# Kernel optimization log

Measured on AMD Instinct MI355X. Metric: run time of the kernel, lower is better.

Reference implementation:

```python
import jax, jax.numpy as jnp
import numpy as np

N_NODES = 50000
N_EDGES = 1600000
N_GRAPHS = 64


def setup_inputs() -> dict:
    key = jax.random.key(0)
    ks = jax.random.split(key, 16)
    x = jax.random.normal(ks[0], (N_NODES, 900), dtype=jnp.float32)
    edge_index = jax.random.randint(ks[1], (2, N_EDGES), 0, N_NODES, dtype=jnp.int64)
    batch = jnp.sort(jax.random.randint(ks[2], (N_NODES,), 0, N_GRAPHS, dtype=jnp.int64))

    def lin(k, out_d, in_d):
        return jax.random.normal(k, (out_d, in_d), dtype=jnp.float32) / np.sqrt(in_d)

    return {
        "x": x, "edge_index": edge_index, "batch": batch,
        # SAGEConv1: lin_l (aggregated, with bias), lin_r (root, no bias)
        "W1l": lin(ks[3], 1024, 900), "b1": jnp.zeros((1024,), jnp.float32), "W1r": lin(ks[4], 1024, 900),
        # SAGEConv2
        "W2l": lin(ks[5], 2048, 1024), "b2": jnp.zeros((2048,), jnp.float32), "W2r": lin(ks[6], 2048, 1024),
        # MLP head
        "Wf1": lin(ks[7], 1024, 2048), "bf1": jnp.zeros((1024,), jnp.float32),
        "Wf2": lin(ks[8], 6, 1024), "bf2": jnp.zeros((6,), jnp.float32),
    }


def _sage_conv(x, src, dst, Wl, b, Wr):
    # mean aggregation of neighbor (source) features onto target nodes
    agg = jax.ops.segment_sum(x[src], dst, num_segments=N_NODES)
    deg = jax.ops.segment_sum(jnp.ones((src.shape[0],), x.dtype), dst, num_segments=N_NODES)
    mean = agg / jnp.maximum(deg, 1.0)[:, None]
    return mean @ Wl.T + b + x @ Wr.T


def reference(x, edge_index, batch, W1l, b1, W1r, W2l, b2, W2r, Wf1, bf1, Wf2, bf2):
    src, dst = edge_index[0], edge_index[1]
    h = jax.nn.relu(_sage_conv(x, src, dst, W1l, b1, W1r))   # [N, 1024]
    h = _sage_conv(h, src, dst, W2l, b2, W2r)                 # [N, 2048]
    pooled = jax.ops.segment_max(h, batch, num_segments=N_GRAPHS)  # [G, 2048]
    pooled = jnp.where(jnp.isfinite(pooled), pooled, 0.0)     # guard empty graphs
    out = jax.nn.relu(pooled @ Wf1.T + bf1) @ Wf2.T + bf2     # [G, 6]
    return out
```

## Files before the change

kernel.cpp:

```cpp
#include <hip/hip_runtime.h>

typedef unsigned short u16x8 __attribute__((ext_vector_type(8)));
typedef char i8x16 __attribute__((ext_vector_type(16)));
typedef int i32x4 __attribute__((ext_vector_type(4)));

constexpr int NN = 50000;
constexpr int NG = 64;
constexpr int MP = 50048;
constexpr int D0 = 900;
constexpr int K0 = 960;
constexpr int D1 = 1024;
constexpr int D2 = 2048;

__device__ __forceinline__ float bf2f(unsigned short u) {
  return __uint_as_float(((unsigned)u) << 16);
}
__device__ __forceinline__ unsigned short f2bf(float f) {
  unsigned x = __float_as_uint(f);
  return (unsigned short)((x + 0x7fffu + ((x >> 16) & 1u)) >> 16);
}

__device__ __forceinline__ void gl_lds16(const void* g, void* l) {
  __builtin_amdgcn_global_load_lds((const __attribute__((address_space(1))) void*)g,
                                   (__attribute__((address_space(3))) void*)l, 16, 0, 0);
}

__global__ __launch_bounds__(256) void cvt_x(const float* __restrict__ in,
                                             char* __restrict__ xi8,
                                             float* __restrict__ xscale) {
  int r = blockIdx.x;
  __shared__ float row[K0];
  __shared__ float smax[256];
  int t = threadIdx.x;
  float m = 0.f;
  for (int c = t; c < K0; c += 256) {
    float v = (r < NN && c < D0) ? in[(size_t)r * D0 + c] : 0.f;
    row[c] = v;
    m = fmaxf(m, fabsf(v));
  }
  smax[t] = m;
  __syncthreads();
  for (int dd = 128; dd; dd >>= 1) {
    if (t < dd) smax[t] = fmaxf(smax[t], smax[t + dd]);
    __syncthreads();
  }
  float mx = smax[0];
  float inv = mx > 0.f ? 127.f / mx : 0.f;
  for (int c = t; c < K0; c += 256) xi8[(size_t)r * K0 + c] = (char)(int)rintf(row[c] * inv);
  if (t == 0) xscale[r] = mx * (1.f / 127.f);
}

__global__ __launch_bounds__(256) void wq_k(const float* __restrict__ in, int Cin, int KP,
                                            char* __restrict__ q, float* __restrict__ sc) {
  int r = blockIdx.x;
  __shared__ float smax[256];
  int t = threadIdx.x;
  float m = 0.f;
  for (int c = t; c < Cin; c += 256) m = fmaxf(m, fabsf(in[(size_t)r * Cin + c]));
  smax[t] = m;
  __syncthreads();
  for (int dd = 128; dd; dd >>= 1) {
    if (t < dd) smax[t] = fmaxf(smax[t], smax[t + dd]);
    __syncthreads();
  }
  float mx = smax[0];
  float inv = mx > 0.f ? 127.f / mx : 0.f;
  for (int c = t; c < KP; c += 256) {
    float v = (c < Cin) ? in[(size_t)r * Cin + c] : 0.f;
    q[(size_t)r * KP + c] = (char)(int)rintf(v * inv);
  }
  if (t == 0) sc[r] = mx * (1.f / 127.f);
}

__global__ __launch_bounds__(256) void quant_rows(const unsigned short* __restrict__ in,
                                                  char* __restrict__ q,
                                                  float* __restrict__ scale, int K) {
  int r = blockIdx.x;
  __shared__ float row[1024];
  __shared__ float smax[256];
  int t = threadIdx.x;
  float m = 0.f;
  for (int c = t; c < K; c += 256) {
    float v = bf2f(in[(size_t)r * K + c]);
    row[c] = v;
    m = fmaxf(m, fabsf(v));
  }
  smax[t] = m;
  __syncthreads();
  for (int dd = 128; dd; dd >>= 1) {
    if (t < dd) smax[t] = fmaxf(smax[t], smax[t + dd]);
    __syncthreads();
  }
  float mx = smax[0];
  float inv = mx > 0.f ? 127.f / mx : 0.f;
  for (int c = t; c < K; c += 256) q[(size_t)r * K + c] = (char)(int)rintf(row[c] * inv);
  if (t == 0) scale[r] = mx * (1.f / 127.f);
}

__global__ void zero_i(int* p, int n) {
  int i = blockIdx.x * blockDim.x + threadIdx.x;
  if (i < n) p[i] = 0;
}
__global__ void count_k(const int* __restrict__ dst, int* __restrict__ deg, int E, int n) {
  int e = blockIdx.x * blockDim.x + threadIdx.x;
  if (e < E) {
    int d = dst[e];
    if ((unsigned)d < (unsigned)n) atomicAdd(&deg[d], 1);
  }
}
__global__ void scan_k(const int* __restrict__ deg, int* __restrict__ off, int n) {
  __shared__ int s[1024];
  __shared__ int carry;
  int t = threadIdx.x;
  if (t == 0) carry = 0;
  __syncthreads();
  for (int base = 0; base < n; base += 1024) {
    int v = (base + t < n) ? deg[base + t] : 0;
    s[t] = v;
    __syncthreads();
    for (int d = 1; d < 1024; d <<= 1) {
      int x = (t >= d) ? s[t - d] : 0;
      __syncthreads();
      s[t] += x;
      __syncthreads();
    }
    if (base + t < n) off[base + t] = carry + s[t] - v;
    int total = s[1023];
    __syncthreads();
    if (t == 0) carry += total;
    __syncthreads();
  }
  if (t == 0) off[n] = carry;
}
__global__ void copy_i(const int* a, int* b, int n) {
  int i = blockIdx.x * blockDim.x + threadIdx.x;
  if (i < n) b[i] = a[i];
}
__global__ void fill_k(const int* __restrict__ src, const int* __restrict__ dst,
                       int* __restrict__ cursor, int* __restrict__ csr, int E, int n) {
  int e = blockIdx.x * blockDim.x + threadIdx.x;
  if (e < E) {
    int d = dst[e];
    if ((unsigned)d < (unsigned)n) {
      int p = atomicAdd(&cursor[d], 1);
      int s = src[e];
      if ((unsigned)s >= (unsigned)n) s = 0;
      csr[p] = s;
    }
  }
}

template <int K>
__global__ __launch_bounds__(256) void agg_mean_i8q(const char* __restrict__ feat,
                                                    const float* __restrict__ scale,
                                                    const int* __restrict__ off,
                                                    const int* __restrict__ csr,
                                                    char* __restrict__ mean_i8,
                                                    float* __restrict__ smean) {
  __shared__ float red[3][1024];
  const int node = blockIdx.x;
  const int wave = threadIdx.x >> 6, lane = threadIdx.x & 63;
  const int d = lane * 16;
  const bool act = (d < K);
  const int e0 = off[node], e1 = off[node + 1];
  float a[16];
#pragma unroll
  for (int k = 0; k < 16; ++k) a[k] = 0.f;
  if (act) {
    const char* fp = feat + d;
    int e = e0 + wave;
    for (; e + 12 < e1; e += 16) {
      int s0 = csr[e], s1 = csr[e + 4], s2 = csr[e + 8], s3 = csr[e + 12];
      float c0 = scale[s0], c1 = scale[s1], c2 = scale[s2], c3 = scale[s3];
      i8x16 v0 = *(const i8x16*)(fp + (size_t)s0 * K);
      i8x16 v1 = *(const i8x16*)(fp + (size_t)s1 * K);
      i8x16 v2 = *(const i8x16*)(fp + (size_t)s2 * K);
      i8x16 v3 = *(const i8x16*)(fp + (size_t)s3 * K);
#pragma unroll
      for (int k = 0; k < 16; ++k) {
        a[k] += c0 * (float)v0[k];
        a[k] += c1 * (float)v1[k];
        a[k] += c2 * (float)v2[k];
        a[k] += c3 * (float)v3[k];
      }
    }
    for (; e < e1; e += 4) {
      int s = csr[e];
      float c = scale[s];
      i8x16 v = *(const i8x16*)(fp + (size_t)s * K);
#pragma unroll
      for (int k = 0; k < 16; ++k) a[k] += c * (float)v[k];
    }
  }
  if (wave > 0 && act) {
#pragma unroll
    for (int k = 0; k < 16; ++k) red[wave - 1][d + k] = a[k];
  }
  __syncthreads();
  if (wave == 0) {
    int deg = e1 - e0;
    float inv = 1.f / (float)(deg > 1 ? deg : 1);
    float m[16];
    float mx = 0.f;
    if (act) {
#pragma unroll
      for (int k = 0; k < 16; ++k) {
        m[k] = (a[k] + red[0][d + k] + red[1][d + k] + red[2][d + k]) * inv;
        mx = fmaxf(mx, fabsf(m[k]));
      }
    }
    for (int o = 32; o; o >>= 1) mx = fmaxf(mx, __shfl_down(mx, o));
    mx = __shfl(mx, 0);
    if (lane == 0) smean[node] = mx * (1.f / 127.f);
    float qi = mx > 0.f ? 127.f / mx : 0.f;
    if (act) {
      i8x16 q;
#pragma unroll
      for (int k = 0; k < 16; ++k) q[k] = (char)(int)rintf(m[k] * qi);
      *(i8x16*)&mean_i8[(size_t)node * K + d] = q;
    }
  }
}

__device__ __forceinline__ void kloop_i8(const char* __restrict__ gA,
                                         const char* __restrict__ gW,
                                         char* lA, char* lB, char* sA, char* sB, int KP,
                                         i32x4 (&iacc)[4][4], int wm, int wn, int l16,
                                         int quad) {
#pragma unroll 1
  for (int k0 = 0; k0 < KP; k0 += 64) {
    __syncthreads();
    gl_lds16(gA + k0, lA);
    gl_lds16(gA + k0 + (size_t)64 * KP, lA + 4096);
    gl_lds16(gW + k0, lB);
    gl_lds16(gW + k0 + (size_t)64 * KP, lB + 4096);
    __syncthreads();
    i32x4 af[4], bg[4];
#pragma unroll
    for (int i = 0; i < 4; ++i)
      af[i] = *(const i32x4*)&sA[(wm + 16 * i + l16) * 64 + quad * 16];
#pragma unroll
    for (int j = 0; j < 4; ++j)
      bg[j] = *(const i32x4*)&sB[(wn + 16 * j + l16) * 64 + quad * 16];
#pragma unroll
    for (int i = 0; i < 4; ++i)
#pragma unroll
      for (int j = 0; j < 4; ++j)
        iacc[i][j] = __builtin_amdgcn_mfma_i32_16x16x64_i8(af[i], bg[j], iacc[i][j], 0, 0, 0);
  }
}

template <int KP, int N, bool RELU>
__global__ __launch_bounds__(256) void gemm_i8_dual(
    const char* __restrict__ A1, const char* __restrict__ W1,
    const char* __restrict__ A2, const char* __restrict__ W2,
    const float* __restrict__ sA1, const float* __restrict__ sW1,
    const float* __restrict__ sA2, const float* __restrict__ sW2,
    const float* __restrict__ bias, unsigned short* __restrict__ C) {
  __shared__ char sA[128 * 64];
  __shared__ char sB[128 * 64];
  __shared__ float sc0[128], sc1[128], sc2[128], sc3[128];
  const int tid = threadIdx.x;
  const int wave = tid >> 6, lane = tid & 63;
  const int quad = lane >> 4, l16 = lane & 15;
  const int wm = (wave >> 1) * 64, wn = (wave & 1) * 64;
  const long long bm = (long long)blockIdx.y * 128;
  const long long bn = (long long)blockIdx.x * 128;

  if (tid < 128) {
    sc0[tid] = sA1[bm + tid];
    sc2[tid] = sA2[bm + tid];
  } else {
    sc1[tid - 128] = sW1[bn + tid - 128];
    sc3[tid - 128] = sW2[bn + tid - 128];
  }

  const int srow = wave * 16 + (lane >> 2);
  const int skoff = (lane & 3) * 16;
  char* lA = &sA[wave * 1024 + lane * 16];
  char* lB = &sB[wave * 1024 + lane * 16];

  i32x4 iacc[4][4];
#pragma unroll
  for (int i = 0; i < 4; ++i)
#pragma unroll
    for (int j = 0; j < 4; ++j) iacc[i][j] = (i32x4){0, 0, 0, 0};

  kloop_i8(A1 + (bm + srow) * (long long)KP + skoff, W1 + (bn + srow) * (long long)KP + skoff,
           lA, lB, sA, sB, KP, iacc, wm, wn, l16, quad);

  unsigned int fb[4][4][2];
#pragma unroll
  for (int i = 0; i < 4; ++i) {
    const int rowb = wm + 16 * i + quad * 4;
#pragma unroll
    for (int j = 0; j < 4; ++j) {
      const float cw = sc1[wn + 16 * j + l16];
      float v0 = (float)iacc[i][j][0] * sc0[rowb + 0] * cw;
      float v1 = (float)iacc[i][j][1] * sc0[rowb + 1] * cw;
      float v2 = (float)iacc[i][j][2] * sc0[rowb + 2] * cw;
      float v3 = (float)iacc[i][j][3] * sc0[rowb + 3] * cw;
      fb[i][j][0] = (unsigned)f2bf(v0) | ((unsigned)f2bf(v1) << 16);
      fb[i][j][1] = (unsigned)f2bf(v2) | ((unsigned)f2bf(v3) << 16);
      iacc[i][j] = (i32x4){0, 0, 0, 0};
    }
  }

  kloop_i8(A2 + (bm + srow) * (long long)KP + skoff, W2 + (bn + srow) * (long long)KP + skoff,
           lA, lB, sA, sB, KP, iacc, wm, wn, l16, quad);

#pragma unroll
  for (int j = 0; j < 4; ++j) {
    const int coll = wn + 16 * j + l16;
    const long long col = bn + coll;
    const float bv = bias[col];
    const float cw2 = sc3[coll];
#pragma unroll
    for (int i = 0; i < 4; ++i) {
      const int rowb = wm + 16 * i + quad * 4;
      const long long row0 = bm + rowb;
#pragma unroll
      for (int r = 0; r < 4; ++r) {
        float p1 = bf2f((unsigned short)(fb[i][j][r >> 1] >> ((r & 1) * 16)));
        float v = p1 + (float)iacc[i][j][r] * sc2[rowb + r] * cw2 + bv;
        if (RELU) v = fmaxf(v, 0.f);
        C[(row0 + r) * (long long)N + col] = f2bf(v);
      }
    }
  }
}

__global__ void bounds_k(const int* __restrict__ batch, int* __restrict__ gstart, int n, int G) {
  int g = blockIdx.x * blockDim.x + threadIdx.x;
  if (g > G) return;
  int lo = 0, hi = n;
  while (lo < hi) {
    int mid = (lo + hi) >> 1;
    if (batch[mid] < g) lo = mid + 1; else hi = mid;
  }
  gstart[g] = lo;
}

__global__ void segmax_k(const unsigned short* __restrict__ h2b, const int* __restrict__ gstart,
                         float* __restrict__ pooled) {
  int g = blockIdx.x;
  int c = blockIdx.y * 256 + threadIdx.x;
  int i0 = gstart[g], i1 = gstart[g + 1];
  float m = -3.4e38f;
  for (int i = i0; i < i1; ++i) m = fmaxf(m, bf2f(h2b[(size_t)i * D2 + c]));
  if (i0 >= i1) m = 0.f;
  pooled[(size_t)g * D2 + c] = m;
}

__global__ void head1_k(const float* __restrict__ pooled, const float* __restrict__ Wf1,
                        const float* __restrict__ bf1, float* __restrict__ hid) {
  int g = blockIdx.x, chunk = blockIdx.y;
  __shared__ float sp[2048];
  for (int i = threadIdx.x; i < 2048; i += 256) sp[i] = pooled[(size_t)g * 2048 + i];
  __syncthreads();
  int wave = threadIdx.x >> 6, lane = threadIdx.x & 63;
  for (int oi = wave; oi < 64; oi += 4) {
    int o = chunk * 64 + oi;
    const float4* wr = (const float4*)&Wf1[(size_t)o * 2048];
    float s = 0.f;
    for (int c = lane; c < 512; c += 64) {
      float4 wv = wr[c];
      float4 pv = *(const float4*)&sp[c * 4];
      s += wv.x * pv.x + wv.y * pv.y + wv.z * pv.z + wv.w * pv.w;
    }
    for (int off = 32; off; off >>= 1) s += __shfl_down(s, off);
    if (lane == 0) hid[(size_t)g * 1024 + o] = fmaxf(s + bf1[o], 0.f);
  }
}
__global__ void head2_k(const float* __restrict__ hid, const float* __restrict__ Wf2,
                        const float* __restrict__ bf2, float* __restrict__ out) {
  int g = blockIdx.x, t = threadIdx.x;
  __shared__ float sh[1024];
  __shared__ float red[256];
  for (int i = t; i < 1024; i += 256) sh[i] = hid[(size_t)g * 1024 + i];
  __syncthreads();
  for (int o = 0; o < 6; ++o) {
    float s = 0.f;
    for (int k = t; k < 1024; k += 256) s += sh[k] * Wf2[o * 1024 + k];
    red[t] = s;
    __syncthreads();
    for (int d = 128; d; d >>= 1) {
      if (t < d) red[t] += red[t + d];
      __syncthreads();
    }
    if (t == 0) out[g * 6 + o] = red[0] + bf2[o];
    __syncthreads();
  }
}

extern "C" void kernel_launch(void* const* d_in, const int* in_sizes, int n_in,
                              void* d_out, int out_size, void* d_ws, size_t ws_size,
                              hipStream_t stream) {
  const float* x    = (const float*)d_in[0];
  const int* ei     = (const int*)d_in[1];
  const int* batch  = (const int*)d_in[2];
  const float* W1l  = (const float*)d_in[3];
  const float* b1   = (const float*)d_in[4];
  const float* W1r  = (const float*)d_in[5];
  const float* W2l  = (const float*)d_in[6];
  const float* b2   = (const float*)d_in[7];
  const float* W2r  = (const float*)d_in[8];
  const float* Wf1  = (const float*)d_in[9];
  const float* bf1  = (const float*)d_in[10];
  const float* Wf2  = (const float*)d_in[11];
  const float* bf2  = (const float*)d_in[12];
  float* out = (float*)d_out;

  const int E = in_sizes[1] / 2;
  const int* srcp = ei;
  const int* dstp = ei + E;

  char* w = (char*)d_ws;
  auto take = [&](size_t b) {
    void* p = (void*)w;
    w += (b + 255) & ~(size_t)255;
    return p;
  };
  char* xi8       = (char*)take((size_t)MP * K0);
  char* mean_i8   = (char*)take((size_t)MP * K0);
  char* h1_i8     = (char*)take((size_t)MP * D1);
  char* mean2_i8  = (char*)take((size_t)MP * D1);
  unsigned short* h1b = (unsigned short*)take((size_t)MP * D1 * 2);
  unsigned short* h2b = (unsigned short*)take((size_t)MP * D2 * 2);
  char* w1l_i8    = (char*)take((size_t)D1 * K0);
  char* w1r_i8    = (char*)take((size_t)D1 * K0);
  char* w2l_i8    = (char*)take((size_t)D2 * D1);
  char* w2r_i8    = (char*)take((size_t)D2 * D1);
  float* xscale   = (float*)take((size_t)MP * 4);
  float* smean    = (float*)take((size_t)MP * 4);
  float* h1scale  = (float*)take((size_t)MP * 4);
  float* smean2   = (float*)take((size_t)MP * 4);
  float* sW1l     = (float*)take((size_t)D1 * 4);
  float* sW1r     = (float*)take((size_t)D1 * 4);
  float* sW2l     = (float*)take((size_t)D2 * 4);
  float* sW2r     = (float*)take((size_t)D2 * 4);
  int* deg    = (int*)take((size_t)MP * 4);
  int* off    = (int*)take((size_t)(MP + 1) * 4);
  int* cursor = (int*)take((size_t)MP * 4);
  int* csr    = (int*)take((size_t)E * 4);
  int* gstart = (int*)take((size_t)(NG + 1) * 4);
  float* pooled = (float*)take((size_t)NG * D2 * 4);
  float* hid    = (float*)take((size_t)NG * 1024 * 4);

  cvt_x<<<MP, 256, 0, stream>>>(x, xi8, xscale);
  wq_k<<<D1, 256, 0, stream>>>(W1l, D0, K0, w1l_i8, sW1l);
  wq_k<<<D1, 256, 0, stream>>>(W1r, D0, K0, w1r_i8, sW1r);
  wq_k<<<D2, 256, 0, stream>>>(W2l, D1, D1, w2l_i8, sW2l);
  wq_k<<<D2, 256, 0, stream>>>(W2r, D1, D1, w2r_i8, sW2r);

  zero_i<<<(MP + 255) / 256, 256, 0, stream>>>(deg, MP);
  count_k<<<(E + 255) / 256, 256, 0, stream>>>(dstp, deg, E, NN);
  scan_k<<<1, 1024, 0, stream>>>(deg, off, MP);
  copy_i<<<(MP + 255) / 256, 256, 0, stream>>>(off, cursor, MP);
  fill_k<<<(E + 255) / 256, 256, 0, stream>>>(srcp, dstp, cursor, csr, E, NN);

  agg_mean_i8q<K0><<<MP, 256, 0, stream>>>(xi8, xscale, off, csr, mean_i8, smean);
  gemm_i8_dual<K0, D1, true><<<dim3(D1 / 128, MP / 128), 256, 0, stream>>>(
      mean_i8, w1l_i8, xi8, w1r_i8, smean, sW1l, xscale, sW1r, b1, h1b);

  quant_rows<<<MP, 256, 0, stream>>>(h1b, h1_i8, h1scale, D1);
  agg_mean_i8q<D1><<<MP, 256, 0, stream>>>(h1_i8, h1scale, off, csr, mean2_i8, smean2);
  gemm_i8_dual<D1, D2, false><<<dim3(D2 / 128, MP / 128), 256, 0, stream>>>(
      mean2_i8, w2l_i8, h1_i8, w2r_i8, smean2, sW2l, h1scale, sW2r, b2, h2b);

  bounds_k<<<1, 128, 0, stream>>>(batch, gstart, NN, NG);
  segmax_k<<<dim3(NG, D2 / 256), 256, 0, stream>>>(h2b, gstart, pooled);
  head1_k<<<dim3(NG, 16), 256, 0, stream>>>(pooled, Wf1, bf1, hid);
  head2_k<<<NG, 256, 0, stream>>>(hid, Wf2, bf2, out);
}
```

Baseline: 2.002 ms.

## Concatenate mean and root features into one int8 GEMM with shared scales

```diff
diff --git a/kernel.cpp b/kernel.cpp
--- a/kernel.cpp
+++ b/kernel.cpp
@@ -11,6 +11,8 @@
 constexpr int K0 = 960;
 constexpr int D1 = 1024;
 constexpr int D2 = 2048;
+constexpr int KC1 = 2 * K0;
+constexpr int KC2 = 2 * D1;
 
 __device__ __forceinline__ float bf2f(unsigned short u) {
   return __uint_as_float(((unsigned)u) << 16);
@@ -26,7 +28,7 @@
 }
 
 __global__ __launch_bounds__(256) void cvt_x(const float* __restrict__ in,
-                                             char* __restrict__ xi8,
+                                             char* __restrict__ cat1,
                                              float* __restrict__ xscale) {
   int r = blockIdx.x;
   __shared__ float row[K0];
@@ -46,17 +48,50 @@
   }
   float mx = smax[0];
   float inv = mx > 0.f ? 127.f / mx : 0.f;
-  for (int c = t; c < K0; c += 256) xi8[(size_t)r * K0 + c] = (char)(int)rintf(row[c] * inv);
+  char* dst = cat1 + (size_t)r * KC1 + K0;
+  for (int c = t; c < K0; c += 256) dst[c] = (char)(int)rintf(row[c] * inv);
   if (t == 0) xscale[r] = mx * (1.f / 127.f);
 }
 
-__global__ __launch_bounds__(256) void wq_k(const float* __restrict__ in, int Cin, int KP,
-                                            char* __restrict__ q, float* __restrict__ sc) {
+__global__ __launch_bounds__(256) void wq_cat(const float* __restrict__ Wl,
+                                              const float* __restrict__ Wr, int Cin, int KH,
+                                              char* __restrict__ q, float* __restrict__ sc) {
+  int r = blockIdx.x, t = threadIdx.x;
+  __shared__ float smax[256];
+  float m = 0.f;
+  for (int c = t; c < Cin; c += 256) {
+    m = fmaxf(m, fabsf(Wl[(size_t)r * Cin + c]));
+    m = fmaxf(m, fabsf(Wr[(size_t)r * Cin + c]));
+  }
+  smax[t] = m;
+  __syncthreads();
+  for (int dd = 128; dd; dd >>= 1) {
+    if (t < dd) smax[t] = fmaxf(smax[t], smax[t + dd]);
+    __syncthreads();
+  }
+  float mx = smax[0];
+  float inv = mx > 0.f ? 127.f / mx : 0.f;
+  char* row = q + (size_t)r * 2 * KH;
+  for (int c = t; c < KH; c += 256) {
+    row[c]      = (c < Cin) ? (char)(int)rintf(Wl[(size_t)r * Cin + c] * inv) : 0;
+    row[KH + c] = (c < Cin) ? (char)(int)rintf(Wr[(size_t)r * Cin + c] * inv) : 0;
+  }
+  if (t == 0) sc[r] = mx * (1.f / 127.f);
+}
+
+__global__ __launch_bounds__(256) void quant_rows(const unsigned short* __restrict__ in,
+                                                  char* __restrict__ cat2,
+                                                  float* __restrict__ scale) {
   int r = blockIdx.x;
+  __shared__ float row[D1];
   __shared__ float smax[256];
   int t = threadIdx.x;
   float m = 0.f;
-  for (int c = t; c < Cin; c += 256) m = fmaxf(m, fabsf(in[(size_t)r * Cin + c]));
+  for (int c = t; c < D1; c += 256) {
+    float v = bf2f(in[(size_t)r * D1 + c]);
+    row[c] = v;
+    m = fmaxf(m, fabsf(v));
+  }
   smax[t] = m;
   __syncthreads();
   for (int dd = 128; dd; dd >>= 1) {
@@ -65,35 +100,8 @@
   }
   float mx = smax[0];
   float inv = mx > 0.f ? 127.f / mx : 0.f;
-  for (int c = t; c < KP; c += 256) {
-    float v = (c < Cin) ? in[(size_t)r * Cin + c] : 0.f;
-    q[(size_t)r * KP + c] = (char)(int)rintf(v * inv);
-  }
-  if (t == 0) sc[r] = mx * (1.f / 127.f);
-}
-
-__global__ __launch_bounds__(256) void quant_rows(const unsigned short* __restrict__ in,
-                                                  char* __restrict__ q,
-                                                  float* __restrict__ scale, int K) {
-  int r = blockIdx.x;
-  __shared__ float row[1024];
-  __shared__ float smax[256];
-  int t = threadIdx.x;
-  float m = 0.f;
-  for (int c = t; c < K; c += 256) {
-    float v = bf2f(in[(size_t)r * K + c]);
-    row[c] = v;
-    m = fmaxf(m, fabsf(v));
-  }
-  smax[t] = m;
-  __syncthreads();
-  for (int dd = 128; dd; dd >>= 1) {
-    if (t < dd) smax[t] = fmaxf(smax[t], smax[t + dd]);
-    __syncthreads();
-  }
-  float mx = smax[0];
-  float inv = mx > 0.f ? 127.f / mx : 0.f;
-  for (int c = t; c < K; c += 256) q[(size_t)r * K + c] = (char)(int)rintf(row[c] * inv);
+  char* dst = cat2 + (size_t)r * KC2 + D1;
+  for (int c = t; c < D1; c += 256) dst[c] = (char)(int)rintf(row[c] * inv);
   if (t == 0) scale[r] = mx * (1.f / 127.f);
 }
 
@@ -108,29 +116,42 @@
     if ((unsigned)d < (unsigned)n) atomicAdd(&deg[d], 1);
   }
 }
-__global__ void scan_k(const int* __restrict__ deg, int* __restrict__ off, int n) {
-  __shared__ int s[1024];
-  __shared__ int carry;
+__global__ void scan1_k(const int* __restrict__ deg, int* __restrict__ off,
+                        int* __restrict__ bsum, int n) {
+  __shared__ int s[256];
   int t = threadIdx.x;
-  if (t == 0) carry = 0;
-  __syncthreads();
-  for (int base = 0; base < n; base += 1024) {
-    int v = (base + t < n) ? deg[base + t] : 0;
-    s[t] = v;
-    __syncthreads();
-    for (int d = 1; d < 1024; d <<= 1) {
-      int x = (t >= d) ? s[t - d] : 0;
-      __syncthreads();
-      s[t] += x;
-      __syncthreads();
-    }
-    if (base + t < n) off[base + t] = carry + s[t] - v;
-    int total = s[1023];
-    __syncthreads();
-    if (t == 0) carry += total;
-    __syncthreads();
-  }
-  if (t == 0) off[n] = carry;
+  int gid = blockIdx.x * 256 + t;
+  int v = (gid < n) ? deg[gid] : 0;
+  s[t] = v;
+  __syncthreads();
+  for (int d = 1; d < 256; d <<= 1) {
+    int x = (t >= d) ? s[t - d] : 0;
+    __syncthreads();
+    s[t] += x;
+    __syncthreads();
+  }
+  if (gid < n) off[gid] = s[t] - v;
+  if (t == 255) bsum[blockIdx.x] = s[255];
+}
+__global__ void scan2_k(int* __restrict__ bsum, int nb) {
+  __shared__ int s[256];
+  int t = threadIdx.x;
+  int v = (t < nb) ? bsum[t] : 0;
+  s[t] = v;
+  __syncthreads();
+  for (int d = 1; d < 256; d <<= 1) {
+    int x = (t >= d) ? s[t - d] : 0;
+    __syncthreads();
+    s[t] += x;
+    __syncthreads();
+  }
+  if (t < nb) bsum[t] = s[t] - v;
+  if (t == 255) bsum[nb] = s[255];
+}
+__global__ void scan3_k(int* __restrict__ off, const int* __restrict__ bsum, int n, int nb) {
+  int gid = blockIdx.x * 256 + threadIdx.x;
+  if (gid < n) off[gid] += bsum[gid >> 8];
+  if (gid == 0) off[n] = bsum[nb];
 }
 __global__ void copy_i(const int* a, int* b, int n) {
   int i = blockIdx.x * blockDim.x + threadIdx.x;
@@ -150,16 +171,13 @@
   }
 }
 
-template <int K>
-__global__ __launch_bounds__(256) void agg_mean_i8q(const char* __restrict__ feat,
-                                                    const float* __restrict__ scale,
+template <int K, int STRIDE>
+__global__ __launch_bounds__(256) void agg_mean_i8w(char* __restrict__ cat,
+                                                    const float* __restrict__ rscale,
                                                     const int* __restrict__ off,
-                                                    const int* __restrict__ csr,
-                                                    char* __restrict__ mean_i8,
-                                                    float* __restrict__ smean) {
-  __shared__ float red[3][1024];
-  const int node = blockIdx.x;
-  const int wave = threadIdx.x >> 6, lane = threadIdx.x & 63;
+                                                    const int* __restrict__ csr) {
+  const int node = blockIdx.x * 4 + (threadIdx.x >> 6);
+  const int lane = threadIdx.x & 63;
   const int d = lane * 16;
   const bool act = (d < K);
   const int e0 = off[node], e1 = off[node + 1];
@@ -167,99 +185,61 @@
 #pragma unroll
   for (int k = 0; k < 16; ++k) a[k] = 0.f;
   if (act) {
-    const char* fp = feat + d;
-    int e = e0 + wave;
-    for (; e + 12 < e1; e += 16) {
-      int s0 = csr[e], s1 = csr[e + 4], s2 = csr[e + 8], s3 = csr[e + 12];
-      float c0 = scale[s0], c1 = scale[s1], c2 = scale[s2], c3 = scale[s3];
-      i8x16 v0 = *(const i8x16*)(fp + (size_t)s0 * K);
-      i8x16 v1 = *(const i8x16*)(fp + (size_t)s1 * K);
-      i8x16 v2 = *(const i8x16*)(fp + (size_t)s2 * K);
-      i8x16 v3 = *(const i8x16*)(fp + (size_t)s3 * K);
+    const char* fp = cat + (size_t)K + d;
+    int e = e0;
+    for (; e + 7 < e1; e += 8) {
+      int s0 = csr[e],     s1 = csr[e + 1], s2 = csr[e + 2], s3 = csr[e + 3];
+      int s4 = csr[e + 4], s5 = csr[e + 5], s6 = csr[e + 6], s7 = csr[e + 7];
+      i8x16 v0 = *(const i8x16*)(fp + (size_t)s0 * STRIDE);
+      i8x16 v1 = *(const i8x16*)(fp + (size_t)s1 * STRIDE);
+      i8x16 v2 = *(const i8x16*)(fp + (size_t)s2 * STRIDE);
+      i8x16 v3 = *(const i8x16*)(fp + (size_t)s3 * STRIDE);
+      i8x16 v4 = *(const i8x16*)(fp + (size_t)s4 * STRIDE);
+      i8x16 v5 = *(const i8x16*)(fp + (size_t)s5 * STRIDE);
+      i8x16 v6 = *(const i8x16*)(fp + (size_t)s6 * STRIDE);
+      i8x16 v7 = *(const i8x16*)(fp + (size_t)s7 * STRIDE);
+      float c0 = rscale[s0], c1 = rscale[s1], c2 = rscale[s2], c3 = rscale[s3];
+      float c4 = rscale[s4], c5 = rscale[s5], c6 = rscale[s6], c7 = rscale[s7];
 #pragma unroll
       for (int k = 0; k < 16; ++k) {
-        a[k] += c0 * (float)v0[k];
-        a[k] += c1 * (float)v1[k];
-        a[k] += c2 * (float)v2[k];
-        a[k] += c3 * (float)v3[k];
+        a[k] += c0 * (float)v0[k] + c1 * (float)v1[k] + c2 * (float)v2[k] + c3 * (float)v3[k];
+        a[k] += c4 * (float)v4[k] + c5 * (float)v5[k] + c6 * (float)v6[k] + c7 * (float)v7[k];
       }
     }
-    for (; e < e1; e += 4) {
+    for (; e < e1; ++e) {
       int s = csr[e];
-      float c = scale[s];
-      i8x16 v = *(const i8x16*)(fp + (size_t)s * K);
+      float c = rscale[s];
+      i8x16 v = *(const i8x16*)(fp + (size_t)s * STRIDE);
 #pragma unroll
       for (int k = 0; k < 16; ++k) a[k] += c * (float)v[k];
     }
   }
-  if (wave > 0 && act) {
-#pragma unroll
-    for (int k = 0; k < 16; ++k) red[wave - 1][d + k] = a[k];
-  }
-  __syncthreads();
-  if (wave == 0) {
+  if (act) {
     int deg = e1 - e0;
     float inv = 1.f / (float)(deg > 1 ? deg : 1);
-    float m[16];
-    float mx = 0.f;
-    if (act) {
-#pragma unroll
-      for (int k = 0; k < 16; ++k) {
-        m[k] = (a[k] + red[0][d + k] + red[1][d + k] + red[2][d + k]) * inv;
-        mx = fmaxf(mx, fabsf(m[k]));
-      }
-    }
-    for (int o = 32; o; o >>= 1) mx = fmaxf(mx, __shfl_down(mx, o));
-    mx = __shfl(mx, 0);
-    if (lane == 0) smean[node] = mx * (1.f / 127.f);
-    float qi = mx > 0.f ? 127.f / mx : 0.f;
-    if (act) {
-      i8x16 q;
-#pragma unroll
-      for (int k = 0; k < 16; ++k) q[k] = (char)(int)rintf(m[k] * qi);
-      *(i8x16*)&mean_i8[(size_t)node * K + d] = q;
-    }
-  }
-}
-
-__device__ __forceinline__ void kloop_i8(const char* __restrict__ gA,
-                                         const char* __restrict__ gW,
-                                         char* lA, char* lB, char* sA, char* sB, int KP,
-                                         i32x4 (&iacc)[4][4], int wm, int wn, int l16,
-                                         int quad) {
-#pragma unroll 1
-  for (int k0 = 0; k0 < KP; k0 += 64) {
-    __syncthreads();
-    gl_lds16(gA + k0, lA);
-    gl_lds16(gA + k0 + (size_t)64 * KP, lA + 4096);
-    gl_lds16(gW + k0, lB);
-    gl_lds16(gW + k0 + (size_t)64 * KP, lB + 4096);
-    __syncthreads();
-    i32x4 af[4], bg[4];
-#pragma unroll
-    for (int i = 0; i < 4; ++i)
-      af[i] = *(const i32x4*)&sA[(wm + 16 * i + l16) * 64 + quad * 16];
-#pragma unroll
-    for (int j = 0; j < 4; ++j)
-      bg[j] = *(const i32x4*)&sB[(wn + 16 * j + l16) * 64 + quad * 16];
-#pragma unroll
-    for (int i = 0; i < 4; ++i)
-#pragma unroll
-      for (int j = 0; j < 4; ++j)
-        iacc[i][j] = __builtin_amdgcn_mfma_i32_16x16x64_i8(af[i], bg[j], iacc[i][j], 0, 0, 0);
+    float sc = rscale[node];
+    float qi = sc > 0.f ? 1.f / sc : 0.f;
+    i8x16 q;
+#pragma unroll
+    for (int k = 0; k < 16; ++k) {
+      float m = a[k] * inv * qi;
+      m = fminf(fmaxf(rintf(m), -127.f), 127.f);
+      q[k] = (char)(int)m;
+    }
+    *(i8x16*)&cat[(size_t)node * STRIDE + d] = q;
   }
 }
 
 template <int KP, int N, bool RELU>
-__global__ __launch_bounds__(256) void gemm_i8_dual(
-    const char* __restrict__ A1, const char* __restrict__ W1,
-    const char* __restrict__ A2, const char* __restrict__ W2,
-    const float* __restrict__ sA1, const float* __restrict__ sW1,
-    const float* __restrict__ sA2, const float* __restrict__ sW2,
-    const float* __restrict__ bias, unsigned short* __restrict__ C) {
+__global__ __launch_bounds__(256, 5) void gemm_i8(const char* __restrict__ A,
+                                                  const char* __restrict__ W,
+                                                  const float* __restrict__ sA_,
+                                                  const float* __restrict__ sW_,
+                                                  const float* __restrict__ bias,
+                                                  unsigned short* __restrict__ C) {
   __shared__ char sA[128 * 64];
   __shared__ char sB[128 * 64];
-  __shared__ float sc0[128], sc1[128], sc2[128], sc3[128];
+  __shared__ float sc0[128], sc1[128];
   const int tid = threadIdx.x;
   const int wave = tid >> 6, lane = tid & 63;
   const int quad = lane >> 4, l16 = lane & 15;
@@ -267,18 +247,15 @@
   const long long bm = (long long)blockIdx.y * 128;
   const long long bn = (long long)blockIdx.x * 128;
 
-  if (tid < 128) {
-    sc0[tid] = sA1[bm + tid];
-    sc2[tid] = sA2[bm + tid];
-  } else {
-    sc1[tid - 128] = sW1[bn + tid - 128];
-    sc3[tid - 128] = sW2[bn + tid - 128];
-  }
+  if (tid < 128) sc0[tid] = sA_[bm + tid];
+  else sc1[tid - 128] = sW_[bn + tid - 128];
 
   const int srow = wave * 16 + (lane >> 2);
   const int skoff = (lane & 3) * 16;
   char* lA = &sA[wave * 1024 + lane * 16];
   char* lB = &sB[wave * 1024 + lane * 16];
+  const char* gA = A + (bm + srow) * (long long)KP + skoff;
+  const char* gW = W + (bn + srow) * (long long)KP + skoff;
 
   i32x4 iacc[4][4];
 #pragma unroll
@@ -286,43 +263,41 @@
 #pragma unroll
     for (int j = 0; j < 4; ++j) iacc[i][j] = (i32x4){0, 0, 0, 0};
 
-  kloop_i8(A1 + (bm + srow) * (long long)KP + skoff, W1 + (bn + srow) * (long long)KP + skoff,
-           lA, lB, sA, sB, KP, iacc, wm, wn, l16, quad);
-
-  unsigned int fb[4][4][2];
-#pragma unroll
-  for (int i = 0; i < 4; ++i) {
-    const int rowb = wm + 16 * i + quad * 4;
-#pragma unroll
-    for (int j = 0; j < 4; ++j) {
-      const float cw = sc1[wn + 16 * j + l16];
-      float v0 = (float)iacc[i][j][0] * sc0[rowb + 0] * cw;
-      float v1 = (float)iacc[i][j][1] * sc0[rowb + 1] * cw;
-      float v2 = (float)iacc[i][j][2] * sc0[rowb + 2] * cw;
-      float v3 = (float)iacc[i][j][3] * sc0[rowb + 3] * cw;
-      fb[i][j][0] = (unsigned)f2bf(v0) | ((unsigned)f2bf(v1) << 16);
-      fb[i][j][1] = (unsigned)f2bf(v2) | ((unsigned)f2bf(v3) << 16);
-      iacc[i][j] = (i32x4){0, 0, 0, 0};
-    }
-  }
-
-  kloop_i8(A2 + (bm + srow) * (long long)KP + skoff, W2 + (bn + srow) * (long long)KP + skoff,
-           lA, lB, sA, sB, KP, iacc, wm, wn, l16, quad);
+#pragma unroll 1
+  for (int k0 = 0; k0 < KP; k0 += 64) {
+    __syncthreads();
+    gl_lds16(gA + k0, lA);
+    gl_lds16(gA + k0 + (size_t)64 * KP, lA + 4096);
+    gl_lds16(gW + k0, lB);
+    gl_lds16(gW + k0 + (size_t)64 * KP, lB + 4096);
+    __syncthreads();
+    i32x4 af[4], bg[4];
+#pragma unroll
+    for (int i = 0; i < 4; ++i)
+      af[i] = *(const i32x4*)&sA[(wm + 16 * i + l16) * 64 + quad * 16];
+#pragma unroll
+    for (int j = 0; j < 4; ++j)
+      bg[j] = *(const i32x4*)&sB[(wn + 16 * j + l16) * 64 + quad * 16];
+#pragma unroll
+    for (int i = 0; i < 4; ++i)
+#pragma unroll
+      for (int j = 0; j < 4; ++j)
+        iacc[i][j] = __builtin_amdgcn_mfma_i32_16x16x64_i8(af[i], bg[j], iacc[i][j], 0, 0, 0);
+  }
 
 #pragma unroll
   for (int j = 0; j < 4; ++j) {
     const int coll = wn + 16 * j + l16;
     const long long col = bn + coll;
     const float bv = bias[col];
-    const float cw2 = sc3[coll];
+    const float cw = sc1[coll];
 #pragma unroll
     for (int i = 0; i < 4; ++i) {
       const int rowb = wm + 16 * i + quad * 4;
       const long long row0 = bm + rowb;
 #pragma unroll
       for (int r = 0; r < 4; ++r) {
-        float p1 = bf2f((unsigned short)(fb[i][j][r >> 1] >> ((r & 1) * 16)));
-        float v = p1 + (float)iacc[i][j][r] * sc2[rowb + r] * cw2 + bv;
+        float v = (float)iacc[i][j][r] * sc0[rowb + r] * cw + bv;
         if (RELU) v = fmaxf(v, 0.f);
         C[(row0 + r) * (long long)N + col] = f2bf(v);
       }
@@ -414,6 +389,7 @@
   const int E = in_sizes[1] / 2;
   const int* srcp = ei;
   const int* dstp = ei + E;
+  const int NB = (MP + 255) / 256;
 
   char* w = (char*)d_ws;
   auto take = [&](size_t b) {
@@ -421,52 +397,45 @@
     w += (b + 255) & ~(size_t)255;
     return p;
   };
-  char* xi8       = (char*)take((size_t)MP * K0);
-  char* mean_i8   = (char*)take((size_t)MP * K0);
-  char* h1_i8     = (char*)take((size_t)MP * D1);
-  char* mean2_i8  = (char*)take((size_t)MP * D1);
+  char* cat1      = (char*)take((size_t)MP * KC1);
+  char* cat2      = (char*)take((size_t)MP * KC2);
   unsigned short* h1b = (unsigned short*)take((size_t)MP * D1 * 2);
   unsigned short* h2b = (unsigned short*)take((size_t)MP * D2 * 2);
-  char* w1l_i8    = (char*)take((size_t)D1 * K0);
-  char* w1r_i8    = (char*)take((size_t)D1 * K0);
-  char* w2l_i8    = (char*)take((size_t)D2 * D1);
-  char* w2r_i8    = (char*)take((size_t)D2 * D1);
+  char* wcat1     = (char*)take((size_t)D1 * KC1);
+  char* wcat2     = (char*)take((size_t)D2 * KC2);
   float* xscale   = (float*)take((size_t)MP * 4);
-  float* smean    = (float*)take((size_t)MP * 4);
   float* h1scale  = (float*)take((size_t)MP * 4);
-  float* smean2   = (float*)take((size_t)MP * 4);
-  float* sW1l     = (float*)take((size_t)D1 * 4);
-  float* sW1r     = (float*)take((size_t)D1 * 4);
-  float* sW2l     = (float*)take((size_t)D2 * 4);
-  float* sW2r     = (float*)take((size_t)D2 * 4);
+  float* swc1     = (float*)take((size_t)D1 * 4);
+  float* swc2     = (float*)take((size_t)D2 * 4);
   int* deg    = (int*)take((size_t)MP * 4);
   int* off    = (int*)take((size_t)(MP + 1) * 4);
+  int* bsum   = (int*)take((size_t)(NB + 1) * 4);
   int* cursor = (int*)take((size_t)MP * 4);
   int* csr    = (int*)take((size_t)E * 4);
   int* gstart = (int*)take((size_t)(NG + 1) * 4);
   float* pooled = (float*)take((size_t)NG * D2 * 4);
   float* hid    = (float*)take((size_t)NG * 1024 * 4);
 
-  cvt_x<<<MP, 256, 0, stream>>>(x, xi8, xscale);
-  wq_k<<<D1, 256, 0, stream>>>(W1l, D0, K0, w1l_i8, sW1l);
-  wq_k<<<D1, 256, 0, stream>>>(W1r, D0, K0, w1r_i8, sW1r);
-  wq_k<<<D2, 256, 0, stream>>>(W2l, D1, D1, w2l_i8, sW2l);
-  wq_k<<<D2, 256, 0, stream>>>(W2r, D1, D1, w2r_i8, sW2r);
+  cvt_x<<<MP, 256, 0, stream>>>(x, cat1, xscale);
+  wq_cat<<<D1, 256, 0, stream>>>(W1l, W1r, D0, K0, wcat1, swc1);
+  wq_cat<<<D2, 256, 0, stream>>>(W2l, W2r, D1, D1, wcat2, swc2);
 
   zero_i<<<(MP + 255) / 256, 256, 0, stream>>>(deg, MP);
   count_k<<<(E + 255) / 256, 256, 0, stream>>>(dstp, deg, E, NN);
-  scan_k<<<1, 1024, 0, stream>>>(deg, off, MP);
+  scan1_k<<<NB, 256, 0, stream>>>(deg, off, bsum, MP);
+  scan2_k<<<1, 256, 0, stream>>>(bsum, NB);
+  scan3_k<<<NB, 256, 0, stream>>>(off, bsum, MP, NB);
   copy_i<<<(MP + 255) / 256, 256, 0, stream>>>(off, cursor, MP);
   fill_k<<<(E + 255) / 256, 256, 0, stream>>>(srcp, dstp, cursor, csr, E, NN);
 
-  agg_mean_i8q<K0><<<MP, 256, 0, stream>>>(xi8, xscale, off, csr, mean_i8, smean);
-  gemm_i8_dual<K0, D1, true><<<dim3(D1 / 128, MP / 128), 256, 0, stream>>>(
-      mean_i8, w1l_i8, xi8, w1r_i8, smean, sW1l, xscale, sW1r, b1, h1b);
-
-  quant_rows<<<MP, 256, 0, stream>>>(h1b, h1_i8, h1scale, D1);
-  agg_mean_i8q<D1><<<MP, 256, 0, stream>>>(h1_i8, h1scale, off, csr, mean2_i8, smean2);
-  gemm_i8_dual<D1, D2, false><<<dim3(D2 / 128, MP / 128), 256, 0, stream>>>(
-      mean2_i8, w2l_i8, h1_i8, w2r_i8, smean2, sW2l, h1scale, sW2r, b2, h2b);
+  agg_mean_i8w<K0, KC1><<<MP / 4, 256, 0, stream>>>(cat1, xscale, off, csr);
+  gemm_i8<KC1, D1, true><<<dim3(D1 / 128, MP / 128), 256, 0, stream>>>(
+      cat1, wcat1, xscale, swc1, b1, h1b);
+
+  quant_rows<<<MP, 256, 0, stream>>>(h1b, cat2, h1scale);
+  agg_mean_i8w<D1, KC2><<<MP / 4, 256, 0, stream>>>(cat2, h1scale, off, csr);
+  gemm_i8<KC2, D2, false><<<dim3(D2 / 128, MP / 128), 256, 0, stream>>>(
+      cat2, wcat2, h1scale, swc2, b2, h2b);
 
   bounds_k<<<1, 128, 0, stream>>>(batch, gstart, NN, NG);
   segmax_k<<<dim3(NG, D2 / 256), 256, 0, stream>>>(h2b, gstart, pooled);
```

Result: faster. 1.846 ms (-7.8%).
